# Kernel optimization log

Hardware: AMD Instinct MI355X
Metric: run time of the kernel (lower is better)

The kernel has to match this reference:

```python
import jax, jax.numpy as jnp
import numpy as np

POS_T = 0.7
NEG_T = 0.3


def setup_inputs() -> dict:
    key = jax.random.key(0)
    k1, k2 = jax.random.split(key)
    pred_boxes = jax.random.uniform(k1, (8, 50000, 4), dtype=jnp.float32)
    gt_boxes = jax.random.uniform(k2, (8, 64, 4), dtype=jnp.float32)
    return {"pred_boxes": pred_boxes, "gt_boxes": gt_boxes}


def _cxcywh_to_xyxy(b):
    cx, cy, w, h = jnp.split(b, 4, axis=-1)
    return jnp.concatenate([cx - 0.5 * w, cy - 0.5 * h, cx + 0.5 * w, cy + 0.5 * h], axis=-1)


def _pairwise_iou(gt_xyxy, pr_xyxy):
    # gt_xyxy: [B,G,4], pr_xyxy: [B,N,4] -> ious [B,G,N]
    gt = gt_xyxy[:, :, None, :]   # [B,G,1,4]
    pr = pr_xyxy[:, None, :, :]   # [B,1,N,4]
    lt = jnp.maximum(gt[..., :2], pr[..., :2])
    rb = jnp.minimum(gt[..., 2:], pr[..., 2:])
    wh = jnp.clip(rb - lt, 0.0)
    inter = wh[..., 0] * wh[..., 1]                                   # [B,G,N]
    area_g = (gt[..., 2] - gt[..., 0]) * (gt[..., 3] - gt[..., 1])    # [B,G,1]
    area_p = (pr[..., 2] - pr[..., 0]) * (pr[..., 3] - pr[..., 1])    # [B,1,N]
    return inter / (area_g + area_p - inter)


def reference(pred_boxes, gt_boxes):
    # Dense-mask equivalent of the original ragged index lists:
    #   pos_mask[b,g,n] = True iff pred n is a positive match for gt g
    #                     (iou > POS_T, plus the per-gt argmax pred)
    #   neg_mask[b,n]   = True iff max_g iou < NEG_T
    ious = _pairwise_iou(_cxcywh_to_xyxy(gt_boxes), _cxcywh_to_xyxy(pred_boxes))  # [B,G,N]
    N = ious.shape[-1]
    best = jnp.argmax(ious, axis=-1)                                   # [B,G]
    argmax_onehot = jnp.arange(N)[None, None, :] == best[..., None]    # [B,G,N]
    pos_mask = (ious > POS_T) | argmax_onehot
    neg_mask = jnp.max(ious, axis=1) < NEG_T                           # [B,N]
    return ious, pos_mask, neg_mask
```

## Files before the change

kernel.cpp:

```cpp
#include <hip/hip_runtime.h>
#include <cstdint>
#include <cstddef>

#define NB 8
#define NG 64
#define NP 50000

__device__ __forceinline__ void opaque(float& x) { asm volatile("" : "+v"(x)); }

__global__ __launch_bounds__(256) void iou_main(
    const float* __restrict__ pred,
    const float* __restrict__ gt,
    float* __restrict__ out_iou,
    float* __restrict__ out_pos,
    float* __restrict__ out_neg)
{
    __shared__ float s_gx0[NG], s_gy0[NG], s_gx1[NG], s_gy1[NG], s_ga[NG];
    const int b = blockIdx.y;
    const int tid = threadIdx.x;

    if (tid < NG) {
        const float4 gb = reinterpret_cast<const float4*>(gt)[b * NG + tid];
        float hw = 0.5f * gb.z, hh = 0.5f * gb.w;
        float x0 = gb.x - hw, y0 = gb.y - hh;
        float x1 = gb.x + hw, y1 = gb.y + hh;
        float ga = (x1 - x0) * (y1 - y0);
        opaque(ga);
        s_gx0[tid] = x0; s_gy0[tid] = y0;
        s_gx1[tid] = x1; s_gy1[tid] = y1;
        s_ga[tid]  = ga;
    }
    __syncthreads();

    const int p = 2 * (blockIdx.x * blockDim.x + tid);
    if (p >= NP) return;

    const float4 pb0 = reinterpret_cast<const float4*>(pred)[(size_t)b * NP + p];
    const float4 pb1 = reinterpret_cast<const float4*>(pred)[(size_t)b * NP + p + 1];

    float hw0 = 0.5f * pb0.z, hh0 = 0.5f * pb0.w;
    const float ax0 = pb0.x - hw0, ay0 = pb0.y - hh0;
    const float ax1 = pb0.x + hw0, ay1 = pb0.y + hh0;
    float pa0 = (ax1 - ax0) * (ay1 - ay0);
    opaque(pa0);

    float hw1 = 0.5f * pb1.z, hh1 = 0.5f * pb1.w;
    const float bx0 = pb1.x - hw1, by0 = pb1.y - hh1;
    const float bx1 = pb1.x + hw1, by1 = pb1.y + hh1;
    float pa1 = (bx1 - bx0) * (by1 - by0);
    opaque(pa1);

    float maxv0 = 0.0f, maxv1 = 0.0f;
    const size_t base = (size_t)b * NG * NP + p;

    #pragma unroll 8
    for (int g = 0; g < NG; ++g) {
        const float gx0 = s_gx0[g], gy0 = s_gy0[g];
        const float gx1 = s_gx1[g], gy1 = s_gy1[g];
        const float ga  = s_ga[g];

        float w0 = fmaxf(fminf(gx1, ax1) - fmaxf(gx0, ax0), 0.0f);
        float h0 = fmaxf(fminf(gy1, ay1) - fmaxf(gy0, ay0), 0.0f);
        float inter0 = w0 * h0;
        opaque(inter0);
        float iou0 = inter0 / ((ga + pa0) - inter0);

        float w1 = fmaxf(fminf(gx1, bx1) - fmaxf(gx0, bx0), 0.0f);
        float h1 = fmaxf(fminf(gy1, by1) - fmaxf(gy0, by0), 0.0f);
        float inter1 = w1 * h1;
        opaque(inter1);
        float iou1 = inter1 / ((ga + pa1) - inter1);

        float2 vi; vi.x = iou0; vi.y = iou1;
        *reinterpret_cast<float2*>(out_iou + base + (size_t)g * NP) = vi;

        float2 vp; vp.x = (iou0 > 0.7f) ? 1.0f : 0.0f;
                   vp.y = (iou1 > 0.7f) ? 1.0f : 0.0f;
        *reinterpret_cast<float2*>(out_pos + base + (size_t)g * NP) = vp;

        maxv0 = fmaxf(maxv0, iou0);
        maxv1 = fmaxf(maxv1, iou1);
    }

    float2 vn; vn.x = (maxv0 < 0.3f) ? 1.0f : 0.0f;
               vn.y = (maxv1 < 0.3f) ? 1.0f : 0.0f;
    *reinterpret_cast<float2*>(out_neg + (size_t)b * NP + p) = vn;
}

__global__ __launch_bounds__(256) void argmax_fix(
    const float* __restrict__ out_iou,
    float* __restrict__ out_pos)
{
    const int row = blockIdx.x;
    const float4* r4 = reinterpret_cast<const float4*>(out_iou + (size_t)row * NP);

    float bv = -1.0f;
    int   bi = 0x7fffffff;
    for (int c = threadIdx.x; c < NP / 4; c += 256) {
        float4 v = r4[c];
        int p = 4 * c;
        if (v.x > bv) { bv = v.x; bi = p; }
        if (v.y > bv) { bv = v.y; bi = p + 1; }
        if (v.z > bv) { bv = v.z; bi = p + 2; }
        if (v.w > bv) { bv = v.w; bi = p + 3; }
    }

    #pragma unroll
    for (int s = 1; s < 64; s <<= 1) {
        float ov = __shfl_xor(bv, s, 64);
        int   oi = __shfl_xor(bi, s, 64);
        if (ov > bv || (ov == bv && oi < bi)) { bv = ov; bi = oi; }
    }

    __shared__ float sv[4];
    __shared__ int   si[4];
    const int wid = threadIdx.x >> 6;
    if ((threadIdx.x & 63) == 0) { sv[wid] = bv; si[wid] = bi; }
    __syncthreads();

    if (threadIdx.x == 0) {
        for (int w = 1; w < 4; ++w)
            if (sv[w] > bv || (sv[w] == bv && si[w] < bi)) { bv = sv[w]; bi = si[w]; }
        out_pos[(size_t)row * NP + bi] = 1.0f;
    }
}

extern "C" void kernel_launch(void* const* d_in, const int* in_sizes, int n_in,
                              void* d_out, int out_size, void* d_ws, size_t ws_size,
                              hipStream_t stream) {
    const float* pred = (const float*)d_in[0];
    const float* gt   = (const float*)d_in[1];
    float* out_iou = (float*)d_out;
    float* out_pos = out_iou + (size_t)NB * NG * NP;
    float* out_neg = out_pos + (size_t)NB * NG * NP;

    dim3 grid1((NP / 2 + 255) / 256, NB);
    iou_main<<<grid1, dim3(256), 0, stream>>>(pred, gt, out_iou, out_pos, out_neg);

    argmax_fix<<<dim3(NB * NG), dim3(256), 0, stream>>>(out_iou, out_pos);
}
```

Before: 60.54 us.

## Fuse per-gt argmax into IoU kernel via packed per-wave partial keys

The IoU kernel now computes a per-wave argmax for each gt row. It packs each result into a 64-bit key (IoU bits plus the inverted index) and writes it to workspace. A small second kernel reduces the 392 partials per row, so the full 102 MB IoU tensor no longer has to be re-read. In exchange the main kernel gains 64 wave reductions per thread and a 64-entry register array, which raises register pressure, and it depends on the workspace being large enough.

```diff
diff --git a/kernel.cpp b/kernel.cpp
--- a/kernel.cpp
+++ b/kernel.cpp
@@ -5,15 +5,22 @@
 #define NB 8
 #define NG 64
 #define NP 50000
+#define NBLK 98
+#define NPART (NBLK * 4)
 
 __device__ __forceinline__ void opaque(float& x) { asm volatile("" : "+v"(x)); }
-
+__device__ __forceinline__ unsigned long long umax64(unsigned long long a, unsigned long long b) {
+    return a > b ? a : b;
+}
+
+template<bool WRITE_KEYS>
 __global__ __launch_bounds__(256) void iou_main(
     const float* __restrict__ pred,
     const float* __restrict__ gt,
     float* __restrict__ out_iou,
     float* __restrict__ out_pos,
-    float* __restrict__ out_neg)
+    float* __restrict__ out_neg,
+    unsigned long long* __restrict__ keys)
 {
     __shared__ float s_gx0[NG], s_gy0[NG], s_gx1[NG], s_gy1[NG], s_ga[NG];
     const int b = blockIdx.y;
@@ -32,11 +39,12 @@
     }
     __syncthreads();
 
-    const int p = 2 * (blockIdx.x * blockDim.x + tid);
-    if (p >= NP) return;
-
-    const float4 pb0 = reinterpret_cast<const float4*>(pred)[(size_t)b * NP + p];
-    const float4 pb1 = reinterpret_cast<const float4*>(pred)[(size_t)b * NP + p + 1];
+    const int p = 2 * (blockIdx.x * 256 + tid);
+    const bool active = p < NP;
+    const int pc = active ? p : 0;
+
+    const float4 pb0 = reinterpret_cast<const float4*>(pred)[(size_t)b * NP + pc];
+    const float4 pb1 = reinterpret_cast<const float4*>(pred)[(size_t)b * NP + pc + 1];
 
     float hw0 = 0.5f * pb0.z, hh0 = 0.5f * pb0.w;
     const float ax0 = pb0.x - hw0, ay0 = pb0.y - hh0;
@@ -51,9 +59,12 @@
     opaque(pa1);
 
     float maxv0 = 0.0f, maxv1 = 0.0f;
-    const size_t base = (size_t)b * NG * NP + p;
-
-    #pragma unroll 8
+    const size_t base = (size_t)b * NG * NP + (size_t)pc;
+
+    float va[NG];
+    unsigned int cm0 = 0, cm1 = 0;
+
+    #pragma unroll
     for (int g = 0; g < NG; ++g) {
         const float gx0 = s_gx0[g], gy0 = s_gy0[g];
         const float gx1 = s_gx1[g], gy1 = s_gy1[g];
@@ -71,23 +82,86 @@
         opaque(inter1);
         float iou1 = inter1 / ((ga + pa1) - inter1);
 
-        float2 vi; vi.x = iou0; vi.y = iou1;
-        *reinterpret_cast<float2*>(out_iou + base + (size_t)g * NP) = vi;
-
-        float2 vp; vp.x = (iou0 > 0.7f) ? 1.0f : 0.0f;
-                   vp.y = (iou1 > 0.7f) ? 1.0f : 0.0f;
-        *reinterpret_cast<float2*>(out_pos + base + (size_t)g * NP) = vp;
-
-        maxv0 = fmaxf(maxv0, iou0);
-        maxv1 = fmaxf(maxv1, iou1);
-    }
-
-    float2 vn; vn.x = (maxv0 < 0.3f) ? 1.0f : 0.0f;
-               vn.y = (maxv1 < 0.3f) ? 1.0f : 0.0f;
-    *reinterpret_cast<float2*>(out_neg + (size_t)b * NP + p) = vn;
-}
-
-__global__ __launch_bounds__(256) void argmax_fix(
+        if (WRITE_KEYS) {
+            va[g] = active ? fmaxf(iou0, iou1) : -1.0f;
+            if (iou1 > iou0) {
+                if (g < 32) cm0 |= 1u << g; else cm1 |= 1u << (g - 32);
+            }
+        }
+
+        if (active) {
+            float2 vi; vi.x = iou0; vi.y = iou1;
+            *reinterpret_cast<float2*>(out_iou + base + (size_t)g * NP) = vi;
+            float2 vp; vp.x = (iou0 > 0.7f) ? 1.0f : 0.0f;
+                       vp.y = (iou1 > 0.7f) ? 1.0f : 0.0f;
+            *reinterpret_cast<float2*>(out_pos + base + (size_t)g * NP) = vp;
+            maxv0 = fmaxf(maxv0, iou0);
+            maxv1 = fmaxf(maxv1, iou1);
+        }
+    }
+
+    if (active) {
+        float2 vn; vn.x = (maxv0 < 0.3f) ? 1.0f : 0.0f;
+                   vn.y = (maxv1 < 0.3f) ? 1.0f : 0.0f;
+        *reinterpret_cast<float2*>(out_neg + (size_t)b * NP + p) = vn;
+    }
+
+    if (WRITE_KEYS) {
+        const int lane = tid & 63;
+        const int wv = tid >> 6;
+        const unsigned int base_p = (unsigned int)(2 * (blockIdx.x * 256 + (tid & ~63)));
+        unsigned long long mykey = 0;
+
+        #pragma unroll
+        for (int g = 0; g < NG; ++g) {
+            float r = va[g];
+            float wmax = r;
+            #pragma unroll
+            for (int s = 1; s < 64; s <<= 1)
+                wmax = fmaxf(wmax, __shfl_xor(wmax, s, 64));
+            unsigned long long key = 0;
+            if (wmax >= 0.0f) {
+                unsigned long long mwin = __ballot(r == wmax);
+                unsigned long long cb   = __ballot((((g < 32) ? cm0 : cm1) >> (g & 31)) & 1u);
+                int wl = __ffsll(mwin) - 1;
+                unsigned int widx = base_p + 2u * (unsigned)wl + (unsigned)((cb >> wl) & 1ull);
+                key = ((unsigned long long)__float_as_uint(wmax) << 32) |
+                      (unsigned long long)(0xFFFFFFFFu - widx);
+            }
+            if (lane == g) mykey = key;
+        }
+        keys[((size_t)b * NG + (size_t)lane) * NPART + (size_t)(blockIdx.x * 4 + wv)] = mykey;
+    }
+}
+
+__global__ __launch_bounds__(256) void pos_fix_keys(
+    const unsigned long long* __restrict__ keys,
+    float* __restrict__ out_pos)
+{
+    const int row = blockIdx.x;
+    const int t = threadIdx.x;
+    const unsigned long long* rk = keys + (size_t)row * NPART;
+
+    unsigned long long k = 0;
+    if (t < NPART)       k = rk[t];
+    if (t + 256 < NPART) k = umax64(k, rk[t + 256]);
+
+    #pragma unroll
+    for (int s = 1; s < 64; s <<= 1)
+        k = umax64(k, __shfl_xor(k, s, 64));
+
+    __shared__ unsigned long long sk[4];
+    if ((t & 63) == 0) sk[t >> 6] = k;
+    __syncthreads();
+
+    if (t == 0) {
+        k = umax64(umax64(sk[0], sk[1]), umax64(sk[2], sk[3]));
+        unsigned int idx = 0xFFFFFFFFu - (unsigned int)(k & 0xFFFFFFFFull);
+        if (idx < NP) out_pos[(size_t)row * NP + idx] = 1.0f;
+    }
+}
+
+__global__ __launch_bounds__(256) void argmax_scan(
     const float* __restrict__ out_iou,
     float* __restrict__ out_pos)
 {
@@ -104,20 +178,17 @@
         if (v.z > bv) { bv = v.z; bi = p + 2; }
         if (v.w > bv) { bv = v.w; bi = p + 3; }
     }
-
     #pragma unroll
     for (int s = 1; s < 64; s <<= 1) {
         float ov = __shfl_xor(bv, s, 64);
         int   oi = __shfl_xor(bi, s, 64);
         if (ov > bv || (ov == bv && oi < bi)) { bv = ov; bi = oi; }
     }
-
     __shared__ float sv[4];
     __shared__ int   si[4];
     const int wid = threadIdx.x >> 6;
     if ((threadIdx.x & 63) == 0) { sv[wid] = bv; si[wid] = bi; }
     __syncthreads();
-
     if (threadIdx.x == 0) {
         for (int w = 1; w < 4; ++w)
             if (sv[w] > bv || (sv[w] == bv && si[w] < bi)) { bv = sv[w]; bi = si[w]; }
@@ -134,8 +205,15 @@
     float* out_pos = out_iou + (size_t)NB * NG * NP;
     float* out_neg = out_pos + (size_t)NB * NG * NP;
 
-    dim3 grid1((NP / 2 + 255) / 256, NB);
-    iou_main<<<grid1, dim3(256), 0, stream>>>(pred, gt, out_iou, out_pos, out_neg);
-
-    argmax_fix<<<dim3(NB * NG), dim3(256), 0, stream>>>(out_iou, out_pos);
-}
+    const size_t keys_bytes = (size_t)NB * NG * NPART * sizeof(unsigned long long);
+    dim3 grid1(NBLK, NB);
+
+    if (ws_size >= keys_bytes) {
+        unsigned long long* keys = (unsigned long long*)d_ws;
+        iou_main<true><<<grid1, dim3(256), 0, stream>>>(pred, gt, out_iou, out_pos, out_neg, keys);
+        pos_fix_keys<<<dim3(NB * NG), dim3(256), 0, stream>>>(keys, out_pos);
+    } else {
+        iou_main<false><<<grid1, dim3(256), 0, stream>>>(pred, gt, out_iou, out_pos, out_neg, nullptr);
+        argmax_scan<<<dim3(NB * NG), dim3(256), 0, stream>>>(out_iou, out_pos);
+    }
+}
```

Measured after the change: 131.8 us. +117.7%, slower.

## Precompute per-gt argmax from recomputed IoUs before the main write pass

Applied to the files above, without the earlier changes.

Adds a pre-pass kernel that recomputes IoUs from the input boxes and reduces per-gt argmax with packed 64-bit keys (IoU bits above inverted index). The main kernel then sets the argmax flag directly while writing the pos mask. This removes the second kernel that re-read the whole 102 MB IoU output to find each argmax. The cost is redundant IoU arithmetic and an extra launch, and the new path depends on the workspace being large enough, falling back to the old path otherwise.

```diff
diff --git a/kernel.cpp b/kernel.cpp
--- a/kernel.cpp
+++ b/kernel.cpp
@@ -5,17 +5,97 @@
 #define NB 8
 #define NG 64
 #define NP 50000
+#define NBLK 98
+#define PCH 6250
+#define NPCH 8
 
 __device__ __forceinline__ void opaque(float& x) { asm volatile("" : "+v"(x)); }
-
+__device__ __forceinline__ unsigned long long umax64(unsigned long long a, unsigned long long b) {
+    return a > b ? a : b;
+}
+
+__global__ __launch_bounds__(256) void argmax_part(
+    const float* __restrict__ pred,
+    const float* __restrict__ gt,
+    unsigned long long* __restrict__ part)
+{
+    __shared__ float s_gx0[8], s_gy0[8], s_gx1[8], s_gy1[8], s_ga[8];
+    const int b  = blockIdx.z;
+    const int gg = blockIdx.y;
+    const int p0 = blockIdx.x * PCH;
+    const int tid = threadIdx.x;
+
+    if (tid < 8) {
+        const float4 gb = reinterpret_cast<const float4*>(gt)[b * NG + gg * 8 + tid];
+        float hw = 0.5f * gb.z, hh = 0.5f * gb.w;
+        float x0 = gb.x - hw, y0 = gb.y - hh;
+        float x1 = gb.x + hw, y1 = gb.y + hh;
+        float ga = (x1 - x0) * (y1 - y0);
+        opaque(ga);
+        s_gx0[tid] = x0; s_gy0[tid] = y0;
+        s_gx1[tid] = x1; s_gy1[tid] = y1;
+        s_ga[tid]  = ga;
+    }
+    __syncthreads();
+
+    unsigned long long k0 = 0, k1 = 0, k2 = 0, k3 = 0, k4 = 0, k5 = 0, k6 = 0, k7 = 0;
+
+    for (int i = tid; i < PCH; i += 256) {
+        const int p = p0 + i;
+        const float4 pb = reinterpret_cast<const float4*>(pred)[(size_t)b * NP + p];
+        float hw = 0.5f * pb.z, hh = 0.5f * pb.w;
+        const float px0 = pb.x - hw, py0 = pb.y - hh;
+        const float px1 = pb.x + hw, py1 = pb.y + hh;
+        float pa = (px1 - px0) * (py1 - py0);
+        opaque(pa);
+
+        const unsigned int ip = 0xFFFFFFFFu - (unsigned int)p;
+        unsigned long long* ks[8] = { &k0,&k1,&k2,&k3,&k4,&k5,&k6,&k7 };
+        #pragma unroll
+        for (int j = 0; j < 8; ++j) {
+            float w = fmaxf(fminf(s_gx1[j], px1) - fmaxf(s_gx0[j], px0), 0.0f);
+            float h = fmaxf(fminf(s_gy1[j], py1) - fmaxf(s_gy0[j], py0), 0.0f);
+            float inter = w * h;
+            opaque(inter);
+            float iou = inter / ((s_ga[j] + pa) - inter);
+            unsigned long long key =
+                ((unsigned long long)__float_as_uint(iou) << 32) | (unsigned long long)ip;
+            *ks[j] = umax64(*ks[j], key);
+        }
+    }
+
+    __shared__ unsigned long long s_part[8][4];
+    const int lane = tid & 63;
+    const int wv = tid >> 6;
+    unsigned long long ka[8] = { k0,k1,k2,k3,k4,k5,k6,k7 };
+    #pragma unroll
+    for (int j = 0; j < 8; ++j) {
+        unsigned long long k = ka[j];
+        #pragma unroll
+        for (int s = 1; s < 64; s <<= 1)
+            k = umax64(k, __shfl_xor(k, s, 64));
+        if (lane == 0) s_part[j][wv] = k;
+    }
+    __syncthreads();
+
+    if (tid < 8) {
+        unsigned long long r = umax64(umax64(s_part[tid][0], s_part[tid][1]),
+                                      umax64(s_part[tid][2], s_part[tid][3]));
+        part[((size_t)b * NG + (size_t)(gg * 8 + tid)) * NPCH + blockIdx.x] = r;
+    }
+}
+
+template<bool USE_AM>
 __global__ __launch_bounds__(256) void iou_main(
     const float* __restrict__ pred,
     const float* __restrict__ gt,
     float* __restrict__ out_iou,
     float* __restrict__ out_pos,
-    float* __restrict__ out_neg)
+    float* __restrict__ out_neg,
+    const unsigned long long* __restrict__ part)
 {
     __shared__ float s_gx0[NG], s_gy0[NG], s_gx1[NG], s_gy1[NG], s_ga[NG];
+    __shared__ unsigned int s_am[NG];
     const int b = blockIdx.y;
     const int tid = threadIdx.x;
 
@@ -29,10 +109,17 @@
         s_gx0[tid] = x0; s_gy0[tid] = y0;
         s_gx1[tid] = x1; s_gy1[tid] = y1;
         s_ga[tid]  = ga;
-    }
-    __syncthreads();
-
-    const int p = 2 * (blockIdx.x * blockDim.x + tid);
+        if (USE_AM) {
+            const unsigned long long* pr = part + ((size_t)b * NG + tid) * NPCH;
+            unsigned long long r = pr[0];
+            #pragma unroll
+            for (int c = 1; c < NPCH; ++c) r = umax64(r, pr[c]);
+            s_am[tid] = 0xFFFFFFFFu - (unsigned int)(r & 0xFFFFFFFFull);
+        }
+    }
+    __syncthreads();
+
+    const int p = 2 * (blockIdx.x * 256 + tid);
     if (p >= NP) return;
 
     const float4 pb0 = reinterpret_cast<const float4*>(pred)[(size_t)b * NP + p];
@@ -51,7 +138,8 @@
     opaque(pa1);
 
     float maxv0 = 0.0f, maxv1 = 0.0f;
-    const size_t base = (size_t)b * NG * NP + p;
+    const size_t base = (size_t)b * NG * NP + (size_t)p;
+    const unsigned int up = (unsigned int)p;
 
     #pragma unroll 8
     for (int g = 0; g < NG; ++g) {
@@ -74,8 +162,15 @@
         float2 vi; vi.x = iou0; vi.y = iou1;
         *reinterpret_cast<float2*>(out_iou + base + (size_t)g * NP) = vi;
 
-        float2 vp; vp.x = (iou0 > 0.7f) ? 1.0f : 0.0f;
-                   vp.y = (iou1 > 0.7f) ? 1.0f : 0.0f;
+        float2 vp;
+        if (USE_AM) {
+            const unsigned int am = s_am[g];
+            vp.x = (iou0 > 0.7f || am == up)      ? 1.0f : 0.0f;
+            vp.y = (iou1 > 0.7f || am == up + 1u) ? 1.0f : 0.0f;
+        } else {
+            vp.x = (iou0 > 0.7f) ? 1.0f : 0.0f;
+            vp.y = (iou1 > 0.7f) ? 1.0f : 0.0f;
+        }
         *reinterpret_cast<float2*>(out_pos + base + (size_t)g * NP) = vp;
 
         maxv0 = fmaxf(maxv0, iou0);
@@ -87,7 +182,7 @@
     *reinterpret_cast<float2*>(out_neg + (size_t)b * NP + p) = vn;
 }
 
-__global__ __launch_bounds__(256) void argmax_fix(
+__global__ __launch_bounds__(256) void argmax_scan(
     const float* __restrict__ out_iou,
     float* __restrict__ out_pos)
 {
@@ -104,20 +199,17 @@
         if (v.z > bv) { bv = v.z; bi = p + 2; }
         if (v.w > bv) { bv = v.w; bi = p + 3; }
     }
-
     #pragma unroll
     for (int s = 1; s < 64; s <<= 1) {
         float ov = __shfl_xor(bv, s, 64);
         int   oi = __shfl_xor(bi, s, 64);
         if (ov > bv || (ov == bv && oi < bi)) { bv = ov; bi = oi; }
     }
-
     __shared__ float sv[4];
     __shared__ int   si[4];
     const int wid = threadIdx.x >> 6;
     if ((threadIdx.x & 63) == 0) { sv[wid] = bv; si[wid] = bi; }
     __syncthreads();
-
     if (threadIdx.x == 0) {
         for (int w = 1; w < 4; ++w)
             if (sv[w] > bv || (sv[w] == bv && si[w] < bi)) { bv = sv[w]; bi = si[w]; }
@@ -134,8 +226,15 @@
     float* out_pos = out_iou + (size_t)NB * NG * NP;
     float* out_neg = out_pos + (size_t)NB * NG * NP;
 
-    dim3 grid1((NP / 2 + 255) / 256, NB);
-    iou_main<<<grid1, dim3(256), 0, stream>>>(pred, gt, out_iou, out_pos, out_neg);
-
-    argmax_fix<<<dim3(NB * NG), dim3(256), 0, stream>>>(out_iou, out_pos);
-}
+    const size_t part_bytes = (size_t)NB * NG * NPCH * sizeof(unsigned long long);
+    dim3 gridA(NBLK, NB);
+
+    if (ws_size >= part_bytes) {
+        unsigned long long* part = (unsigned long long*)d_ws;
+        argmax_part<<<dim3(NPCH, NG / 8, NB), dim3(256), 0, stream>>>(pred, gt, part);
+        iou_main<true><<<gridA, dim3(256), 0, stream>>>(pred, gt, out_iou, out_pos, out_neg, part);
+    } else {
+        iou_main<false><<<gridA, dim3(256), 0, stream>>>(pred, gt, out_iou, out_pos, out_neg, nullptr);
+        argmax_scan<<<dim3(NB * NG), dim3(256), 0, stream>>>(out_iou, out_pos);
+    }
+}
```

After: 71.79 us. 1.19x slower.
